# Kernel tuning notes

Measured on AMD Instinct MI355X. Metric: run time of the kernel, lower is better.

## Reference

```python
import jax, jax.numpy as jnp
import numpy as np

THR = 0.6
EPS = 1e-12


def _mlp(x, w1, b1, w2, b2):
    # Linear -> ReLU -> (Dropout eval = identity) -> Linear
    return jax.nn.relu(x @ w1 + b1) @ w2 + b2


def setup_inputs() -> dict:
    B, H, D = 16384, 1024, 300
    key = jax.random.key(0)
    ks = jax.random.split(key, 32)
    s = 0.02
    inp = {
        'brics': jax.random.normal(ks[0], (B, H), jnp.float32),
        'function_group': jax.random.normal(ks[1], (B, H), jnp.float32),
        'pharmacophore': jax.random.normal(ks[2], (B, H), jnp.float32),
        # fingerprint encoders (brics / function_group / pharmacophore)
        'bw1': jax.random.normal(ks[3], (H, D), jnp.float32) * s,
        'bb1': jnp.zeros((D,), jnp.float32),
        'bw2': jax.random.normal(ks[4], (D, H), jnp.float32) * s,
        'bb2': jnp.zeros((H,), jnp.float32),
        'fw1': jax.random.normal(ks[5], (H, D), jnp.float32) * s,
        'fb1': jnp.zeros((D,), jnp.float32),
        'fw2': jax.random.normal(ks[6], (D, H), jnp.float32) * s,
        'fb2': jnp.zeros((H,), jnp.float32),
        'pw1': jax.random.normal(ks[7], (H, D), jnp.float32) * s,
        'pb1': jnp.zeros((D,), jnp.float32),
        'pw2': jax.random.normal(ks[8], (D, H), jnp.float32) * s,
        'pb2': jnp.zeros((H,), jnp.float32),
        # weight generator: Linear(3H, 3)
        'wg_W': jax.random.normal(ks[9], (3 * H, 3), jnp.float32) * s,
        'wg_b': jnp.zeros((3,), jnp.float32),
        # enhancement layer: Linear(H, H) + sigmoid
        'enh_W': jax.random.normal(ks[10], (H, H), jnp.float32) * s,
        'enh_b': jnp.zeros((H,), jnp.float32),
        # fusion layer: Linear(2H, H)
        'fus_W': jax.random.normal(ks[11], (2 * H, H), jnp.float32) * s,
        'fus_b': jnp.zeros((H,), jnp.float32),
    }
    return inp


def reference(brics, function_group, pharmacophore,
              bw1, bb1, bw2, bb2,
              fw1, fb1, fw2, fb2,
              pw1, pb1, pw2, pb2,
              wg_W, wg_b, enh_W, enh_b, fus_W, fus_b):
    B, H = brics.shape
    eb = _mlp(brics, bw1, bb1, bw2, bb2)            # [B,H]
    ef = _mlp(function_group, fw1, fb1, fw2, fb2)   # [B,H]
    ep = _mlp(pharmacophore, pw1, pb1, pw2, pb2)    # [B,H]

    E = jnp.stack([eb, ef, ep], axis=1)             # [B,3,H]
    En = E / jnp.maximum(jnp.linalg.norm(E, axis=-1, keepdims=True), EPS)

    # three unordered pairs (0,1),(0,2),(1,2); softmax-weighted sum is
    # permutation invariant, so the original python sort is a no-op.
    ii = jnp.array([0, 0, 1])
    jj = jnp.array([1, 2, 2])
    Ei, Ej = E[:, ii], E[:, jj]                     # [B,3,H]
    Eni, Enj = En[:, ii], En[:, jj]
    sim = jnp.sum(Eni * Enj, axis=-1)               # [B,3] cosine sims
    keep = sim > THR                                # pairs above threshold

    elem_mask = (Eni * Enj > THR).astype(E.dtype)   # [B,3,H]
    cf = 0.5 * (Ei + Ej) * elem_mask                # candidate common feats

    w = jax.nn.softmax(jnp.where(keep, sim, -1e9), axis=-1)  # [B,3]
    wsum = jnp.einsum('bp,bph->bh', w, cf)
    mean_fp = jnp.mean(E, axis=1)
    any_kept = jnp.any(keep, axis=-1, keepdims=True)
    common = jnp.where(any_kept, wsum, mean_fp)     # [B,H]

    all_cat = jnp.concatenate([eb, ef, ep], axis=1)          # [B,3H]
    fp_w = jax.nn.softmax(all_cat @ wg_W + wg_b, axis=1)     # [B,3]
    weighted_fp_sum = jnp.einsum('bk,bkh->bh', fp_w, E)

    enh = jax.nn.sigmoid(common @ enh_W + enh_b)
    enhanced_common = common * enh

    fused = jnp.concatenate([weighted_fp_sum, enhanced_common], axis=1) @ fus_W + fus_b
    return fused
```

## Files before the change

### kernel.cpp

```cpp
#include <hip/hip_runtime.h>
#include <stdint.h>


typedef __attribute__((ext_vector_type(8))) __bf16 bf16x8;
typedef __attribute__((ext_vector_type(8))) short short8;
typedef __attribute__((ext_vector_type(4))) float floatx4;

__device__ __forceinline__ uint16_t f2bf(float f) {
  __bf16 h = (__bf16)f;
  return __builtin_bit_cast(uint16_t, h);
}
__device__ __forceinline__ float bf2f(uint16_t h) {
  union { uint32_t u; float f; } v; v.u = ((uint32_t)h) << 16;
  return v.f;
}
__device__ __forceinline__ short8 pack8(float4 a, float4 b) {
  union { __bf16 h[8]; short8 s; } u;
  u.h[0] = (__bf16)a.x; u.h[1] = (__bf16)a.y; u.h[2] = (__bf16)a.z; u.h[3] = (__bf16)a.w;
  u.h[4] = (__bf16)b.x; u.h[5] = (__bf16)b.y; u.h[6] = (__bf16)b.z; u.h[7] = (__bf16)b.w;
  return u.s;
}
__device__ __forceinline__ void gload16(const void* g, void* l) {
  __builtin_amdgcn_global_load_lds(
      (const __attribute__((address_space(1))) void*)g,
      (__attribute__((address_space(3))) void*)l, 16, 0, 0);
}

__global__ void cfe_transpose_all(const float* __restrict__ bw1, const float* __restrict__ fw1,
                                  const float* __restrict__ pw1, const float* __restrict__ bw2,
                                  const float* __restrict__ fw2, const float* __restrict__ pw2,
                                  const float* __restrict__ enhW, const float* __restrict__ fusW,
                                  uint16_t* __restrict__ W1T, uint16_t* __restrict__ W2T,
                                  uint16_t* __restrict__ ENHT, uint16_t* __restrict__ FUST) {
  int bid = blockIdx.x;
  const float* src; uint16_t* dst; int K, N, Kpad, Npad, bx, by;
  if (bid < 1152) {
    int z = bid / 384, t = bid % 384; bx = t % 32; by = t / 32;
    src = (z == 0) ? bw1 : ((z == 1) ? fw1 : pw1); dst = W1T + (long)z * 384 * 1024;
    K = 1024; N = 300; Kpad = 1024; Npad = 384;
  } else if (bid < 2112) {
    bid -= 1152; int z = bid / 320, t = bid % 320; bx = t % 10; by = t / 10;
    src = (z == 0) ? bw2 : ((z == 1) ? fw2 : pw2); dst = W2T + (long)z * 1024 * 320;
    K = 300; N = 1024; Kpad = 320; Npad = 1024;
  } else if (bid < 3136) {
    bid -= 2112; bx = bid % 32; by = bid / 32;
    src = enhW; dst = ENHT; K = 1024; N = 1024; Kpad = 1024; Npad = 1024;
  } else {
    bid -= 3136; bx = bid % 64; by = bid / 64;
    src = fusW; dst = FUST; K = 2048; N = 1024; Kpad = 2048; Npad = 1024;
  }
  __shared__ float tile[32][33];
  const int tx = threadIdx.x & 31;
  const int ty = threadIdx.x >> 5;
  const int k0 = bx * 32;
  const int n0 = by * 32;
#pragma unroll
  for (int i = 0; i < 4; i++) {
    int k = k0 + ty + 8 * i;
    int n = n0 + tx;
    tile[ty + 8 * i][tx] = (k < K && n < N) ? src[(long)k * N + n] : 0.f;
  }
  __syncthreads();
#pragma unroll
  for (int i = 0; i < 4; i++) {
    int n = n0 + ty + 8 * i;
    int k = k0 + tx;
    if (n < Npad && k < Kpad) dst[(long)n * Kpad + k] = f2bf(tile[tx][ty + 8 * i]);
  }
}

template <int MODE, int AF32>
__global__ void cfe_gemm128(const void* __restrict__ A0, const void* __restrict__ A1,
                            const void* __restrict__ A2, int lda,
                            const uint16_t* __restrict__ Bt, long sBz, int ldb,
                            void* __restrict__ C, long sCz, int ldc, int colofs,
                            const float* __restrict__ bias0,
                            const float* __restrict__ bias1,
                            const float* __restrict__ bias2, int biasN,
                            const uint16_t* __restrict__ common, int K) {
  const int z = blockIdx.z;
  const void* Av = (z == 0) ? A0 : ((z == 1) ? A1 : A2);
  Bt += (long)z * sBz;
  const float* bias = (z == 0) ? bias0 : ((z == 1) ? bias1 : bias2);

  const int gx = gridDim.x;
  const int lin = blockIdx.y * gx + blockIdx.x;
  const int P = (gx * gridDim.y) >> 3;
  const int v = (lin & 7) * P + (lin >> 3);
  const long bm = (long)(v / gx) * 128;
  const long bn = (long)(v % gx) * 128;

  const int tid = threadIdx.x;
  const int wave = tid >> 6;
  const int lane = tid & 63;
  const int wm = wave >> 1;
  const int wn = wave & 1;

  __shared__ __attribute__((aligned(16))) uint16_t As[128 * 32];
  __shared__ __attribute__((aligned(16))) uint16_t Bs[128 * 32];

  floatx4 acc[4][4];
#pragma unroll
  for (int i = 0; i < 4; i++)
#pragma unroll
    for (int j = 0; j < 4; j++) acc[i][j] = (floatx4){0.f, 0.f, 0.f, 0.f};

  const int lrow = lane >> 2;
  const int lcol = (lane & 3) * 8;
  const uint16_t* Bp = Bt + (bn + wave * 32 + lrow) * (long)ldb + lcol;
  uint16_t* BsW0 = &Bs[(wave * 32) * 32];
  uint16_t* BsW1 = &Bs[(wave * 32 + 16) * 32];
  const uint16_t* Ap = nullptr;
  uint16_t* AsW0 = &As[(wave * 32) * 32];
  uint16_t* AsW1 = &As[(wave * 32 + 16) * 32];
  const float* ApF0 = nullptr;
  const float* ApF1 = nullptr;
  short8* AsF0 = (short8*)&As[(wave * 32 + lrow) * 32 + lcol];
  short8* AsF1 = (short8*)&As[(wave * 32 + 16 + lrow) * 32 + lcol];
  if constexpr (AF32) {
    ApF0 = (const float*)Av + (bm + wave * 32 + lrow) * (long)lda + lcol;
    ApF1 = ApF0 + 16 * (long)lda;
  } else {
    Ap = (const uint16_t*)Av + (bm + wave * 32 + lrow) * (long)lda + lcol;
  }

  const int fr = lane & 15;
  const int fq = lane >> 4;
  const uint16_t* ArBase = &As[(wm * 64 + fr) * 32 + fq * 8];
  const uint16_t* BrBase = &Bs[(wn * 64 + fr) * 32 + fq * 8];

  float4 f0, f1, f2, f3;
  if constexpr (AF32) {
    f0 = *(const float4*)(ApF0);
    f1 = *(const float4*)(ApF0 + 4);
    f2 = *(const float4*)(ApF1);
    f3 = *(const float4*)(ApF1 + 4);
  }

  for (int k0 = 0; k0 < K; k0 += 32) {
    if constexpr (AF32) {
      gload16(Bp + k0, BsW0);
      gload16(Bp + 16 * (long)ldb + k0, BsW1);
      *AsF0 = pack8(f0, f1);
      *AsF1 = pack8(f2, f3);
    } else {
      gload16(Ap + k0, AsW0);
      gload16(Ap + 16 * (long)lda + k0, AsW1);
      gload16(Bp + k0, BsW0);
      gload16(Bp + 16 * (long)ldb + k0, BsW1);
    }
    __syncthreads();

    if constexpr (AF32) {
      if (k0 + 32 < K) {
        f0 = *(const float4*)(ApF0 + k0 + 32);
        f1 = *(const float4*)(ApF0 + k0 + 36);
        f2 = *(const float4*)(ApF1 + k0 + 32);
        f3 = *(const float4*)(ApF1 + k0 + 36);
      }
    }

    short8 a[4], b[4];
#pragma unroll
    for (int mi = 0; mi < 4; mi++) a[mi] = *(const short8*)(ArBase + mi * 16 * 32);
#pragma unroll
    for (int ni = 0; ni < 4; ni++) b[ni] = *(const short8*)(BrBase + ni * 16 * 32);
#pragma unroll
    for (int mi = 0; mi < 4; mi++)
#pragma unroll
      for (int ni = 0; ni < 4; ni++)
        acc[mi][ni] = __builtin_amdgcn_mfma_f32_16x16x32_bf16(
            __builtin_bit_cast(bf16x8, a[mi]), __builtin_bit_cast(bf16x8, b[ni]),
            acc[mi][ni], 0, 0, 0);
    __syncthreads();
  }

#pragma unroll
  for (int mi = 0; mi < 4; mi++) {
    long row = bm + wm * 64 + mi * 16 + fq * 4;
#pragma unroll
    for (int ni = 0; ni < 4; ni++) {
      long col = bn + wn * 64 + ni * 16 + fr;
      float bv = (col < biasN) ? bias[col] : 0.f;
#pragma unroll
      for (int r = 0; r < 4; r++) {
        float vv = acc[mi][ni][r] + bv;
        long idx = (row + r) * (long)ldc + colofs + col;
        if constexpr (MODE == 0) {
          ((uint16_t*)C)[(long)z * sCz + idx] = f2bf(fmaxf(vv, 0.f));
        } else if constexpr (MODE == 1) {
          ((uint16_t*)C)[(long)z * sCz + idx] = f2bf(vv);
        } else if constexpr (MODE == 2) {
          float c = bf2f(common[(row + r) * 1024 + col]);
          float s = 1.f / (1.f + __expf(-vv));
          ((uint16_t*)C)[idx] = f2bf(c * s);
        } else {
          ((float*)C)[idx] = vv;
        }
      }
    }
  }
}

__global__ void cfe_pointwise_kernel(const uint16_t* __restrict__ E,
                                     const float* __restrict__ wgW,
                                     const float* __restrict__ wgb,
                                     uint16_t* __restrict__ commonb,
                                     uint16_t* __restrict__ fusedA) {
  const int row = blockIdx.x;
  const int tid = threadIdx.x;
  const long ES = 16384L * 1024;
  const long base = (long)row * 1024 + tid * 4;

  ushort4 u0 = *(const ushort4*)(E + base);
  ushort4 u1 = *(const ushort4*)(E + ES + base);
  ushort4 u2 = *(const ushort4*)(E + 2 * ES + base);
  float eb[4] = {bf2f(u0.x), bf2f(u0.y), bf2f(u0.z), bf2f(u0.w)};
  float ef[4] = {bf2f(u1.x), bf2f(u1.y), bf2f(u1.z), bf2f(u1.w)};
  float ep[4] = {bf2f(u2.x), bf2f(u2.y), bf2f(u2.z), bf2f(u2.w)};

  float vals[9];
#pragma unroll
  for (int i = 0; i < 9; i++) vals[i] = 0.f;
#pragma unroll
  for (int j = 0; j < 4; j++) {
    int h = tid * 4 + j;
    vals[0] += eb[j] * eb[j];
    vals[1] += ef[j] * ef[j];
    vals[2] += ep[j] * ep[j];
    vals[3] += eb[j] * ef[j];
    vals[4] += eb[j] * ep[j];
    vals[5] += ef[j] * ep[j];
#pragma unroll
    for (int c = 0; c < 3; c++)
      vals[6 + c] += eb[j] * wgW[(long)h * 3 + c] +
                     ef[j] * wgW[(long)(1024 + h) * 3 + c] +
                     ep[j] * wgW[(long)(2048 + h) * 3 + c];
  }

#pragma unroll
  for (int i = 0; i < 9; i++) {
    float v = vals[i];
    for (int off = 32; off; off >>= 1) v += __shfl_down(v, off);
    vals[i] = v;
  }
  __shared__ float red[4][9];
  if ((tid & 63) == 0) {
#pragma unroll
    for (int i = 0; i < 9; i++) red[tid >> 6][i] = vals[i];
  }
  __syncthreads();
  float tot[9];
#pragma unroll
  for (int i = 0; i < 9; i++)
    tot[i] = red[0][i] + red[1][i] + red[2][i] + red[3][i];

  const float EPSF = 1e-12f;
  float nb = fmaxf(sqrtf(tot[0]), EPSF);
  float nf = fmaxf(sqrtf(tot[1]), EPSF);
  float np_ = fmaxf(sqrtf(tot[2]), EPSF);
  float s01 = tot[3] / (nb * nf);
  float s02 = tot[4] / (nb * np_);
  float s12 = tot[5] / (nf * np_);
  bool k01 = s01 > 0.6f, k02 = s02 > 0.6f, k12 = s12 > 0.6f;
  bool any = k01 | k02 | k12;
  float z0 = k01 ? s01 : -1e9f;
  float z1 = k02 ? s02 : -1e9f;
  float z2 = k12 ? s12 : -1e9f;
  float zm = fmaxf(z0, fmaxf(z1, z2));
  float w0 = __expf(z0 - zm), w1 = __expf(z1 - zm), w2 = __expf(z2 - zm);
  float wsum = w0 + w1 + w2;
  w0 /= wsum; w1 /= wsum; w2 /= wsum;

  float g0 = tot[6] + wgb[0], g1 = tot[7] + wgb[1], g2 = tot[8] + wgb[2];
  float gm = fmaxf(g0, fmaxf(g1, g2));
  float f0 = __expf(g0 - gm), f1 = __expf(g1 - gm), f2 = __expf(g2 - gm);
  float fs = f0 + f1 + f2;
  f0 /= fs; f1 /= fs; f2 /= fs;

  float inb = 1.f / nb, inf_ = 1.f / nf, inp = 1.f / np_;
  ushort4 co, wf;
  uint16_t cov[4], wfv[4];
#pragma unroll
  for (int j = 0; j < 4; j++) {
    float b = eb[j], f = ef[j], p = ep[j];
    float nbv = b * inb, nfv = f * inf_, npv = p * inp;
    float c01 = (nbv * nfv > 0.6f) ? 0.5f * (b + f) : 0.f;
    float c02 = (nbv * npv > 0.6f) ? 0.5f * (b + p) : 0.f;
    float c12 = (nfv * npv > 0.6f) ? 0.5f * (f + p) : 0.f;
    float ws = w0 * c01 + w1 * c02 + w2 * c12;
    float cm = any ? ws : (b + f + p) * (1.f / 3.f);
    float wfs = f0 * b + f1 * f + f2 * p;
    cov[j] = f2bf(cm);
    wfv[j] = f2bf(wfs);
  }
  co.x = cov[0]; co.y = cov[1]; co.z = cov[2]; co.w = cov[3];
  wf.x = wfv[0]; wf.y = wfv[1]; wf.z = wfv[2]; wf.w = wfv[3];
  *(ushort4*)(commonb + base) = co;
  *(ushort4*)(fusedA + (long)row * 2048 + tid * 4) = wf;
}

extern "C" void kernel_launch(void* const* d_in, const int* in_sizes, int n_in,
                              void* d_out, int out_size, void* d_ws, size_t ws_size,
                              hipStream_t stream) {
  (void)in_sizes; (void)n_in; (void)out_size; (void)ws_size;
  const float* brics = (const float*)d_in[0];
  const float* fg    = (const float*)d_in[1];
  const float* ph    = (const float*)d_in[2];
  const float* bw1 = (const float*)d_in[3];  const float* bb1 = (const float*)d_in[4];
  const float* bw2 = (const float*)d_in[5];  const float* bb2 = (const float*)d_in[6];
  const float* fw1 = (const float*)d_in[7];  const float* fb1 = (const float*)d_in[8];
  const float* fw2 = (const float*)d_in[9];  const float* fb2 = (const float*)d_in[10];
  const float* pw1 = (const float*)d_in[11]; const float* pb1 = (const float*)d_in[12];
  const float* pw2 = (const float*)d_in[13]; const float* pb2 = (const float*)d_in[14];
  const float* wgW = (const float*)d_in[15]; const float* wgb = (const float*)d_in[16];
  const float* enhW = (const float*)d_in[17]; const float* enhb = (const float*)d_in[18];
  const float* fusW = (const float*)d_in[19]; const float* fusb = (const float*)d_in[20];
  float* out = (float*)d_out;

  uint16_t* EB   = (uint16_t*)d_ws;
  uint16_t* FA   = EB + 3L * 16384 * 1024;
  uint16_t* W1T  = FA + 16384L * 2048;
  uint16_t* W2T  = W1T + 3L * 384 * 1024;
  uint16_t* ENHT = W2T + 3L * 1024 * 320;
  uint16_t* FUST = ENHT + 1024L * 1024;
  uint16_t* YB   = (uint16_t*)d_out;
  uint16_t* COM  = (uint16_t*)d_out;

  cfe_transpose_all<<<5184, 256, 0, stream>>>(
      bw1, fw1, pw1, bw2, fw2, pw2, enhW, fusW, W1T, W2T, ENHT, FUST);

  cfe_gemm128<0, 1><<<dim3(3, 128, 3), 256, 0, stream>>>(
      brics, fg, ph, 1024, W1T, 384L * 1024, 1024,
      YB, 16384L * 384, 384, 0, bb1, fb1, pb1, 300, nullptr, 1024);

  cfe_gemm128<1, 0><<<dim3(8, 128, 3), 256, 0, stream>>>(
      YB, YB + 16384L * 384, YB + 2 * 16384L * 384, 384, W2T, 1024L * 320, 320,
      EB, 16384L * 1024, 1024, 0, bb2, fb2, pb2, 1024, nullptr, 320);

  cfe_pointwise_kernel<<<16384, 256, 0, stream>>>(EB, wgW, wgb, COM, FA);

  cfe_gemm128<2, 0><<<dim3(8, 128, 1), 256, 0, stream>>>(
      COM, COM, COM, 1024, ENHT, 0, 1024,
      FA, 0, 2048, 1024, enhb, enhb, enhb, 1024, COM, 1024);

  cfe_gemm128<3, 0><<<dim3(8, 128, 1), 256, 0, stream>>>(
      FA, FA, FA, 2048, FUST, 0, 2048,
      out, 0, 1024, 0, fusb, fusb, fusb, 1024, nullptr, 2048);
}
```

Baseline: 541.0 us.

## Stage fp32 A tiles via direct-to-LDS loads and swizzle LDS layouts

For the fp32-activation GEMM path, A tiles are now copied straight into LDS as fp32 with global_load_lds instead of being register-prefetched and packed to bf16 before the store. The bf16 conversion moves to the fragment read after the barrier. Both the A and B LDS tiles use an XOR swizzle on column groups to reduce bank conflicts on fragment reads. This doubles the A LDS footprint and drops the register prefetch overlap of the next A tile, and it adds conversion work to the inner loop.

```diff
diff --git a/kernel.cpp b/kernel.cpp
--- a/kernel.cpp
+++ b/kernel.cpp
@@ -96,7 +96,7 @@
   const int wm = wave >> 1;
   const int wn = wave & 1;
 
-  __shared__ __attribute__((aligned(16))) uint16_t As[128 * 32];
+  __shared__ __attribute__((aligned(16))) uint16_t As[AF32 ? 128 * 64 : 128 * 32];
   __shared__ __attribute__((aligned(16))) uint16_t Bs[128 * 32];
 
   floatx4 acc[4][4];
@@ -106,65 +106,66 @@
     for (int j = 0; j < 4; j++) acc[i][j] = (floatx4){0.f, 0.f, 0.f, 0.f};
 
   const int lrow = lane >> 2;
-  const int lcol = (lane & 3) * 8;
-  const uint16_t* Bp = Bt + (bn + wave * 32 + lrow) * (long)ldb + lcol;
+  const int lcolB = (((lane & 3) ^ ((lrow >> 1) & 3)) * 8);
+  const uint16_t* Bp = Bt + (bn + wave * 32 + lrow) * (long)ldb + lcolB;
   uint16_t* BsW0 = &Bs[(wave * 32) * 32];
   uint16_t* BsW1 = &Bs[(wave * 32 + 16) * 32];
   const uint16_t* Ap = nullptr;
   uint16_t* AsW0 = &As[(wave * 32) * 32];
   uint16_t* AsW1 = &As[(wave * 32 + 16) * 32];
-  const float* ApF0 = nullptr;
-  const float* ApF1 = nullptr;
-  short8* AsF0 = (short8*)&As[(wave * 32 + lrow) * 32 + lcol];
-  short8* AsF1 = (short8*)&As[(wave * 32 + 16 + lrow) * 32 + lcol];
+  if constexpr (!AF32) {
+    Ap = (const uint16_t*)Av + (bm + wave * 32 + lrow) * (long)lda + lcolB;
+  }
+
+  const float* ApS = nullptr;
+  char* AsB = nullptr;
   if constexpr (AF32) {
-    ApF0 = (const float*)Av + (bm + wave * 32 + lrow) * (long)lda + lcol;
-    ApF1 = ApF0 + 16 * (long)lda;
-  } else {
-    Ap = (const uint16_t*)Av + (bm + wave * 32 + lrow) * (long)lda + lcol;
+    const int r_in = lane >> 3;
+    const int gpos = (lane & 7) >> 1;
+    const int halfp = lane & 1;
+    const int scol = ((gpos ^ (r_in & 3)) << 3) | ((halfp ^ ((r_in >> 2) & 1)) << 2);
+    ApS = (const float*)Av + (bm + wave * 32 + r_in) * (long)lda + scol;
+    AsB = (char*)As + (wave * 32) * 128;
   }
 
   const int fr = lane & 15;
   const int fq = lane >> 4;
-  const uint16_t* ArBase = &As[(wm * 64 + fr) * 32 + fq * 8];
-  const uint16_t* BrBase = &Bs[(wn * 64 + fr) * 32 + fq * 8];
-
-  float4 f0, f1, f2, f3;
-  if constexpr (AF32) {
-    f0 = *(const float4*)(ApF0);
-    f1 = *(const float4*)(ApF0 + 4);
-    f2 = *(const float4*)(ApF1);
-    f3 = *(const float4*)(ApF1 + 4);
-  }
+  const int swr = (fr >> 1) & 3;
+  const uint16_t* ArBase = &As[(wm * 64 + fr) * 32 + (fq ^ swr) * 8];
+  const uint16_t* BrBase = &Bs[(wn * 64 + fr) * 32 + (fq ^ swr) * 8];
+  const int ga = fq ^ (fr & 3);
+  const int hb = (fr >> 2) & 1;
+  const float* AfBase = (const float*)As + (wm * 64 + fr) * 32 + ga * 8;
 
   for (int k0 = 0; k0 < K; k0 += 32) {
     if constexpr (AF32) {
-      gload16(Bp + k0, BsW0);
-      gload16(Bp + 16 * (long)ldb + k0, BsW1);
-      *AsF0 = pack8(f0, f1);
-      *AsF1 = pack8(f2, f3);
+      gload16(ApS + k0, AsB);
+      gload16(ApS + 8 * (long)lda + k0, AsB + 1024);
+      gload16(ApS + 16 * (long)lda + k0, AsB + 2048);
+      gload16(ApS + 24 * (long)lda + k0, AsB + 3072);
     } else {
       gload16(Ap + k0, AsW0);
       gload16(Ap + 16 * (long)lda + k0, AsW1);
-      gload16(Bp + k0, BsW0);
-      gload16(Bp + 16 * (long)ldb + k0, BsW1);
     }
+    gload16(Bp + k0, BsW0);
+    gload16(Bp + 16 * (long)ldb + k0, BsW1);
     __syncthreads();
 
+    short8 a[4], b[4];
     if constexpr (AF32) {
-      if (k0 + 32 < K) {
-        f0 = *(const float4*)(ApF0 + k0 + 32);
-        f1 = *(const float4*)(ApF0 + k0 + 36);
-        f2 = *(const float4*)(ApF1 + k0 + 32);
-        f3 = *(const float4*)(ApF1 + k0 + 36);
+#pragma unroll
+      for (int mi = 0; mi < 4; mi++) {
+        const float* Af = AfBase + mi * 512;
+        float4 lo = *(const float4*)(Af + hb * 4);
+        float4 hi = *(const float4*)(Af + (hb ^ 1) * 4);
+        a[mi] = pack8(lo, hi);
       }
+    } else {
+#pragma unroll
+      for (int mi = 0; mi < 4; mi++) a[mi] = *(const short8*)(ArBase + mi * 512);
     }
-
-    short8 a[4], b[4];
-#pragma unroll
-    for (int mi = 0; mi < 4; mi++) a[mi] = *(const short8*)(ArBase + mi * 16 * 32);
-#pragma unroll
-    for (int ni = 0; ni < 4; ni++) b[ni] = *(const short8*)(BrBase + ni * 16 * 32);
+#pragma unroll
+    for (int ni = 0; ni < 4; ni++) b[ni] = *(const short8*)(BrBase + ni * 512);
 #pragma unroll
     for (int mi = 0; mi < 4; mi++)
 #pragma unroll
```

Result: slower. 562.0 us (+3.9%).
